# Kernel tuning notes

Measured on AMD Instinct MI355X. Metric: run time of the kernel, lower is better.

Reference implementation:

```python
import jax, jax.numpy as jnp
import numpy as np

B, V, FIN, H = 200, 40, 16, 128
NSW = 12          # switch edges
NE = 40           # regular edges
M = NE + NSW      # 52 total edges
MLP_HID = 1024
OUT = M + V + NSW # 104


def _build_graph():
    rng = np.random.default_rng(0)
    pairs = set()
    while len(pairs) < M:
        i, j = map(int, rng.integers(0, V, 2))
        if i < j:
            pairs.add((i, j))
    pairs = sorted(pairs)
    reg = np.array(pairs[:NE], np.int64)   # (NE,2)
    sw = np.array(pairs[NE:], np.int64)    # (NSW,2) row-major sorted, matches torch.nonzero order
    edges = np.concatenate([reg, sw], 0)   # switch edges last, matching graph_topo layout
    A = np.zeros((V, M), np.float32)
    A[edges[:, 0], np.arange(M)] = 1.0
    A[edges[:, 1], np.arange(M)] = -1.0
    return reg, sw, A


def setup_inputs():
    key = jax.random.key(0)
    ks = jax.random.split(key, 16)
    reg, sw, A = _build_graph()
    ei = jnp.broadcast_to(jnp.asarray(reg.T)[None], (B, 2, NE))
    si = jnp.broadcast_to(jnp.asarray(sw.T)[None], (B, 2, NSW))

    def w(k, shp, fan):
        return jax.random.normal(k, shp, jnp.float32) / np.sqrt(fan)

    return {
        'x_mod': jax.random.normal(ks[0], (B, V, FIN), jnp.float32),
        'ei': ei, 'si': si, 'A_inc': jnp.asarray(A),
        'embed': w(ks[1], (2, FIN), 1.0),
        'WU0': w(ks[2], (FIN, H), FIN), 'WV0': w(ks[3], (FIN, H), FIN),
        'WA0': w(ks[4], (FIN, H), FIN), 'WB0': w(ks[5], (FIN, H), FIN),
        'WC0': w(ks[6], (FIN, H), FIN),
        'WU1': w(ks[7], (H, H), H), 'WV1': w(ks[8], (H, H), H),
        'WA1': w(ks[9], (H, H), H), 'WB1': w(ks[10], (H, H), H),
        'WC1': w(ks[11], (H, H), H),
        'W1': w(ks[12], ((NSW + V) * H, MLP_HID), (NSW + V) * H),
        'b1': jnp.zeros((MLP_HID,), jnp.float32),
        'W2': w(ks[13], (MLP_HID, OUT), MLP_HID),
        'b2': jnp.zeros((OUT,), jnp.float32),
    }


def _layer(x, s, adj, smask, WU, WV, WA, WB, WC, residual):
    Ux = x @ WU
    Vx = x @ WV
    # gate features over dense VxV switch grid: e_ij = A s_ij + B x_i + C x_j
    e = jnp.einsum('bijf,fh->bijh', s, WA) + (x @ WB)[:, :, None, :] + (x @ WC)[:, None, :, :]
    gates = jax.nn.sigmoid(e) * smask[..., None]
    msg_edges = jnp.einsum('bij,bjh->bih', adj, Vx)   # regular-edge aggregation
    msg_sw = jnp.einsum('bijh,bjh->bih', gates, Vx)   # gated switch aggregation
    xh = jax.nn.relu(Ux + msg_edges + msg_sw)
    sh = jax.nn.relu(e)
    if residual:
        xh = x + xh
        sh = s + sh
    return xh, sh


def reference(x_mod, ei, si, A_inc, embed, WU0, WV0, WA0, WB0, WC0,
              WU1, WV1, WA1, WB1, WC1, W1, b1, W2, b2):
    i_sw, j_sw = si[0, 0], si[0, 1]   # switch indices (shared across batch)
    i_e, j_e = ei[0, 0], ei[0, 1]
    S = jnp.zeros((V, V), bool).at[i_sw, j_sw].set(True)   # upper-tri switch mask
    smask = jnp.broadcast_to(S, (B, V, V)).astype(x_mod.dtype)
    s0 = embed[S.astype(jnp.int32)]                        # (V,V,FIN) edge embedding
    s = jnp.broadcast_to(s0[None], (B, V, V, FIN))
    adj1 = jnp.zeros((V, V), x_mod.dtype).at[i_e, j_e].set(1.0)
    adj = jnp.broadcast_to((adj1 + adj1.T)[None], (B, V, V))
    x, s = _layer(x_mod, s, adj, smask, WU0, WV0, WA0, WB0, WC0, residual=False)
    x, s = _layer(x, s, adj, smask, WU1, WV1, WA1, WB1, WC1, residual=True)
    switches = s[:, i_sw, j_sw, :]                         # (B,NSW,H) irregular gather (torch.nonzero path)
    mlp_in = jnp.concatenate([switches.reshape(B, -1), x.reshape(B, -1)], axis=1)
    out = jax.nn.relu(mlp_in @ W1 + b1) @ W2 + b2          # (B,OUT)
    p_switch = jax.nn.sigmoid(out[:, -NSW:])
    graph_topo = jnp.ones((B, M), out.dtype).at[:, M - NSW:].set(p_switch)
    v = out[:, M:M + V].at[:, 0].set(1.0)
    p_fc = graph_topo * out[:, :M]
    q_fc = graph_topo * (v @ A_inc)                        # per-edge voltage difference flow
    pg = x_mod[:, :, 0] + jnp.einsum('vm,bm->bv', A_inc, p_fc)  # power balance completion
    qg = x_mod[:, :, 1] + jnp.einsum('vm,bm->bv', A_inc, q_fc)
    z = jnp.concatenate([p_fc, v, graph_topo], axis=1)     # (B, 2M+V)
    zc = jnp.concatenate([q_fc, pg, qg], axis=1)           # (B, M+2V)
    return z, zc
```

## Files before the change

kernel.cpp:

```cpp
#include <hip/hip_runtime.h>
#include <math.h>

#define B       200
#define V       40
#define FIN     16
#define H       128
#define NSW     12
#define NE      40
#define M       52
#define MLP_HID 1024
#define OUTD    104
#define MLP_IN  6656
#define ZDIM    144
#define ZCDIM   132
#define NCH     13
#define X1LD    136

typedef __attribute__((ext_vector_type(8))) short bf16x8;
typedef __attribute__((ext_vector_type(4))) float f32x4;

__device__ __forceinline__ float sigmoidf(float x) {
    return 1.0f / (1.0f + expf(-x));
}
__device__ __forceinline__ unsigned short f2b(float x) {
    unsigned int u = __float_as_uint(x);
    u += 0x7fffu + ((u >> 16) & 1u);
    return (unsigned short)(u >> 16);
}
__device__ __forceinline__ float b2f(unsigned short s) {
    return __uint_as_float(((unsigned int)s) << 16);
}

__global__ __launch_bounds__(256) void k_prep(const float* __restrict__ W1,
        const float* __restrict__ WU, const float* __restrict__ WV,
        const float* __restrict__ WB, const float* __restrict__ WC,
        const float* __restrict__ W2,
        unsigned short* __restrict__ W1t, unsigned short* __restrict__ Wt512,
        unsigned short* __restrict__ W2t) {
    int tid = threadIdx.x;
    if (blockIdx.x < 208) {
        int k0 = blockIdx.x * 32, n0 = blockIdx.y * 32;
        __shared__ float tile[32][33];
        int c = tid & 31, r8 = tid >> 5;
#pragma unroll
        for (int i = 0; i < 4; ++i) {
            int r = r8 + i * 8;
            tile[r][c] = W1[(size_t)(k0 + r) * MLP_HID + n0 + c];
        }
        __syncthreads();
#pragma unroll
        for (int i = 0; i < 4; ++i) {
            int rr = r8 + i * 8;
            W1t[(size_t)(n0 + rr) * MLP_IN + k0 + c] = f2b(tile[c][rr]);
        }
    } else if (blockIdx.x == 208) {
        int base = (blockIdx.y * 256 + tid) * 8;
#pragma unroll
        for (int i = 0; i < 8; ++i) {
            int o = base + i;
            int col = o >> 7, f = o & 127;
            int m = col >> 7, h = col & 127;
            const float* Ws = (m == 0) ? WU : (m == 1) ? WV : (m == 2) ? WB : WC;
            Wt512[o] = f2b(Ws[f * H + h]);
        }
    } else {
        for (int o = blockIdx.y * 4096 + tid; o < blockIdx.y * 4096 + 4096; o += 256) {
            int col = o >> 10, k = o & 1023;
            W2t[o] = (col < OUTD) ? f2b(W2[(size_t)k * OUTD + col]) : (unsigned short)0;
        }
    }
}

__global__ __launch_bounds__(512) void k_gnn(const float* __restrict__ x,
        const int* __restrict__ ei, const int* __restrict__ si,
        const float* __restrict__ embed,
        const float* __restrict__ WU0, const float* __restrict__ WV0,
        const float* __restrict__ WB0, const float* __restrict__ WC0,
        const float* __restrict__ WA0, const float* __restrict__ WA1,
        const unsigned short* __restrict__ Wt512,
        unsigned short* __restrict__ Abf) {
    int b = blockIdx.x;
    int tid = threadIdx.x;
    __shared__ unsigned short uvbc[V * 512];
    __shared__ float msg[4][V][H];
    __shared__ unsigned short x1l[48 * X1LD];
    __shared__ unsigned short e0s[NSW * H];
    __shared__ float xs[V * FIN];
    __shared__ float sA1l[NSW * H];

    for (int i = tid; i < V * FIN; i += 512) xs[i] = x[(size_t)b * V * FIN + i];
    __syncthreads();

    int h = tid & 127, sub = tid >> 7;

    {
        int m = sub;
        const float* Wm = (m == 0) ? WU0 : (m == 1) ? WV0 : (m == 2) ? WB0 : WC0;
        float w[FIN];
#pragma unroll
        for (int f = 0; f < FIN; ++f) w[f] = Wm[f * H + h];
        for (int r = 0; r < V; ++r) {
            float acc = 0.f;
#pragma unroll
            for (int f = 0; f < FIN; ++f) acc += xs[r * FIN + f] * w[f];
            uvbc[r * 512 + tid] = f2b(acc);
        }
    }
    for (int i = 0; i < V; ++i) msg[sub][i][h] = 0.f;
    __syncthreads();

    float sA0 = 0.f;
#pragma unroll
    for (int f = 0; f < FIN; ++f) sA0 += embed[FIN + f] * WA0[f * H + h];

    for (int e = sub * 10; e < sub * 10 + 10; ++e) {
        int i = ei[e], j = ei[NE + e];
        msg[sub][i][h] += b2f(uvbc[j * 512 + 128 + h]);
        msg[sub][j][h] += b2f(uvbc[i * 512 + 128 + h]);
    }
    for (int k = sub * 3; k < sub * 3 + 3; ++k) {
        int i = si[k], j = si[NSW + k];
        float e0 = sA0 + b2f(uvbc[i * 512 + 256 + h]) + b2f(uvbc[j * 512 + 384 + h]);
        float g = sigmoidf(e0);
        msg[sub][i][h] += g * b2f(uvbc[j * 512 + 128 + h]);
        e0s[k * H + h] = f2b(fmaxf(e0, 0.f));
    }
    __syncthreads();

    for (int i = sub * 10; i < sub * 10 + 10; ++i) {
        float v = b2f(uvbc[i * 512 + h]) + msg[0][i][h] + msg[1][i][h] + msg[2][i][h] + msg[3][i][h];
        x1l[i * X1LD + h] = f2b(fmaxf(v, 0.f));
    }
    for (int i = 40 + sub; i < 48; i += 4) x1l[i * X1LD + h] = 0;
    for (int o = tid; o < NSW * H; o += 512) {
        int k = o >> 7, hh = o & 127;
        float acc = 0.f;
#pragma unroll 8
        for (int f = 0; f < H; ++f) acc += b2f(e0s[k * H + f]) * WA1[f * H + hh];
        sA1l[o] = acc;
    }
    __syncthreads();

    {
        int lane = tid & 63, wvid = tid >> 6;
        int n0w = wvid * 64;
        int lr = lane & 15, lk = lane >> 4;
        f32x4 acc[3][4];
#pragma unroll
        for (int rf = 0; rf < 3; ++rf)
#pragma unroll
            for (int cf = 0; cf < 4; ++cf) acc[rf][cf] = (f32x4){0.f, 0.f, 0.f, 0.f};

#pragma unroll
        for (int kk = 0; kk < 4; ++kk) {
            int kseg = kk * 32 + lk * 8;
            bf16x8 af0 = *(const bf16x8*)&x1l[(0 * 16 + lr) * X1LD + kseg];
            bf16x8 af1 = *(const bf16x8*)&x1l[(1 * 16 + lr) * X1LD + kseg];
            bf16x8 af2 = *(const bf16x8*)&x1l[(2 * 16 + lr) * X1LD + kseg];
#pragma unroll
            for (int cf = 0; cf < 4; ++cf) {
                int col = n0w + cf * 16 + lr;
                bf16x8 bf = *(const bf16x8*)&Wt512[col * 128 + kseg];
                acc[0][cf] = __builtin_amdgcn_mfma_f32_16x16x32_bf16(af0, bf, acc[0][cf], 0, 0, 0);
                acc[1][cf] = __builtin_amdgcn_mfma_f32_16x16x32_bf16(af1, bf, acc[1][cf], 0, 0, 0);
                acc[2][cf] = __builtin_amdgcn_mfma_f32_16x16x32_bf16(af2, bf, acc[2][cf], 0, 0, 0);
            }
        }
#pragma unroll
        for (int rf = 0; rf < 3; ++rf)
#pragma unroll
            for (int cf = 0; cf < 4; ++cf)
#pragma unroll
                for (int r = 0; r < 4; ++r) {
                    int row = rf * 16 + lk * 4 + r;
                    if (row < V) uvbc[row * 512 + n0w + cf * 16 + lr] = f2b(acc[rf][cf][r]);
                }
    }
    for (int i = 0; i < V; ++i) msg[sub][i][h] = 0.f;
    __syncthreads();

    for (int e = sub * 10; e < sub * 10 + 10; ++e) {
        int i = ei[e], j = ei[NE + e];
        msg[sub][i][h] += b2f(uvbc[j * 512 + 128 + h]);
        msg[sub][j][h] += b2f(uvbc[i * 512 + 128 + h]);
    }
    for (int k = sub * 3; k < sub * 3 + 3; ++k) {
        int i = si[k], j = si[NSW + k];
        float e1 = sA1l[k * H + h] + b2f(uvbc[i * 512 + 256 + h]) + b2f(uvbc[j * 512 + 384 + h]);
        float g = sigmoidf(e1);
        msg[sub][i][h] += g * b2f(uvbc[j * 512 + 128 + h]);
        float s1 = b2f(e0s[k * H + h]);
        Abf[(size_t)b * MLP_IN + k * H + h] = f2b(s1 + fmaxf(e1, 0.f));
    }
    __syncthreads();
    for (int i = sub * 10; i < sub * 10 + 10; ++i) {
        float xh = b2f(uvbc[i * 512 + h]) + msg[0][i][h] + msg[1][i][h] + msg[2][i][h] + msg[3][i][h];
        float x2 = b2f(x1l[i * X1LD + h]) + fmaxf(xh, 0.f);
        Abf[(size_t)b * MLP_IN + NSW * H + i * H + h] = f2b(x2);
    }
}

template<int MODE>
__global__ __launch_bounds__(256) void k_gemm(const unsigned short* __restrict__ A,
        const unsigned short* __restrict__ Bt, void* __restrict__ Cout,
        int K, int nk, int ldc) {
    int tid = threadIdx.x;
    int lane = tid & 63, wv = tid >> 6;
    int wr = (wv >> 1) * 32, wc = (wv & 1) * 32;
    int n0 = blockIdx.x * 64, m0 = blockIdx.y * 64;
    size_t kbase = (size_t)blockIdx.z * nk * 32;

    __shared__ __align__(16) unsigned short a_lds[64 * 40];
    __shared__ __align__(16) unsigned short b_lds[64 * 40];

    f32x4 acc00 = {0,0,0,0}, acc01 = {0,0,0,0}, acc10 = {0,0,0,0}, acc11 = {0,0,0,0};

    int srow = tid >> 2, sseg = tid & 3;
    const int4* gA = (const int4*)(A + (size_t)(m0 + srow) * K + kbase + sseg * 8);
    const int4* gB = (const int4*)(Bt + (size_t)(n0 + srow) * K + kbase + sseg * 8);
    int lws = srow * 40 + sseg * 8;

    int a_off = (wr + (lane & 15)) * 40 + (lane >> 4) * 8;
    int b_off = (wc + (lane & 15)) * 40 + (lane >> 4) * 8;

    int4 ra = gA[0], rb = gB[0];
    for (int kk = 0; kk < nk; ++kk) {
        *(int4*)&a_lds[lws] = ra;
        *(int4*)&b_lds[lws] = rb;
        __syncthreads();
        if (kk + 1 < nk) { ra = gA[(kk + 1) * 4]; rb = gB[(kk + 1) * 4]; }
        bf16x8 a0 = *(const bf16x8*)&a_lds[a_off];
        bf16x8 a1 = *(const bf16x8*)&a_lds[a_off + 16 * 40];
        bf16x8 b0 = *(const bf16x8*)&b_lds[b_off];
        bf16x8 b1 = *(const bf16x8*)&b_lds[b_off + 16 * 40];
        acc00 = __builtin_amdgcn_mfma_f32_16x16x32_bf16(a0, b0, acc00, 0, 0, 0);
        acc01 = __builtin_amdgcn_mfma_f32_16x16x32_bf16(a0, b1, acc01, 0, 0, 0);
        acc10 = __builtin_amdgcn_mfma_f32_16x16x32_bf16(a1, b0, acc10, 0, 0, 0);
        acc11 = __builtin_amdgcn_mfma_f32_16x16x32_bf16(a1, b1, acc11, 0, 0, 0);
        __syncthreads();
    }

    int crow = (lane >> 4) * 4;
    int ccol = lane & 15;
    int row0 = m0 + wr + crow, row1 = row0 + 16;
    int col0 = n0 + wc + ccol, col1 = col0 + 16;
    if (MODE == 1) {
        unsigned short* dst = (unsigned short*)Cout;
#pragma unroll
        for (int r = 0; r < 4; ++r) {
            dst[(size_t)(row0 + r) * ldc + col0] = f2b(acc00[r]);
            dst[(size_t)(row0 + r) * ldc + col1] = f2b(acc01[r]);
            dst[(size_t)(row1 + r) * ldc + col0] = f2b(acc10[r]);
            dst[(size_t)(row1 + r) * ldc + col1] = f2b(acc11[r]);
        }
    } else {
        float* dst = (float*)Cout + (size_t)blockIdx.z * (gridDim.y * 64) * ldc;
#pragma unroll
        for (int r = 0; r < 4; ++r) {
            dst[(size_t)(row0 + r) * ldc + col0] = acc00[r];
            dst[(size_t)(row0 + r) * ldc + col1] = acc01[r];
            dst[(size_t)(row1 + r) * ldc + col0] = acc10[r];
            dst[(size_t)(row1 + r) * ldc + col1] = acc11[r];
        }
    }
}

__global__ void k_mred(const float* __restrict__ partial, const float* __restrict__ b1,
                       unsigned short* __restrict__ hiddenb) {
    int i = blockIdx.x * 256 + threadIdx.x;
    float s = b1[i & (MLP_HID - 1)];
#pragma unroll
    for (int z = 0; z < NCH; ++z) s += partial[(size_t)z * 256 * MLP_HID + i];
    hiddenb[i] = f2b(fmaxf(s, 0.f));
}

__global__ __launch_bounds__(128) void k_fin(const float* __restrict__ partial2,
        const float* __restrict__ b2, const float* __restrict__ A,
        const float* __restrict__ x_mod, float* __restrict__ outp) {
    int b = blockIdx.x;
    int tid = threadIdx.x;
    __shared__ float o[OUTD];
    __shared__ float gt[M], vv[V], pfc[M], qfc[M];

    if (tid < OUTD) {
        float s = b2[tid];
#pragma unroll
        for (int z = 0; z < 4; ++z) s += partial2[(size_t)z * 256 * 128 + b * 128 + tid];
        o[tid] = s;
    }
    __syncthreads();

    if (tid < M) {
        float g = (tid < M - NSW) ? 1.0f : sigmoidf(o[M + V + (tid - (M - NSW))]);
        gt[tid] = g;
        pfc[tid] = g * o[tid];
    }
    if (tid < V) vv[tid] = (tid == 0) ? 1.0f : o[M + tid];
    __syncthreads();

    if (tid < M) {
        float acc = 0.f;
        for (int x = 0; x < V; ++x) acc += vv[x] * A[x * M + tid];
        qfc[tid] = gt[tid] * acc;
    }
    __syncthreads();

    float* zb = outp + (size_t)b * ZDIM;
    if (tid < M) zb[tid] = pfc[tid];
    if (tid < V) zb[M + tid] = vv[tid];
    if (tid < M) zb[M + V + tid] = gt[tid];

    float* zcb = outp + (size_t)B * ZDIM + (size_t)b * ZCDIM;
    if (tid < M) zcb[tid] = qfc[tid];
    if (tid < V) {
        float accp = 0.f, accq = 0.f;
        for (int m = 0; m < M; ++m) {
            float a = A[tid * M + m];
            accp += a * pfc[m];
            accq += a * qfc[m];
        }
        zcb[M + tid]     = x_mod[(size_t)(b * V + tid) * FIN + 0] + accp;
        zcb[M + V + tid] = x_mod[(size_t)(b * V + tid) * FIN + 1] + accq;
    }
}

extern "C" void kernel_launch(void* const* d_in, const int* in_sizes, int n_in,
                              void* d_out, int out_size, void* d_ws, size_t ws_size,
                              hipStream_t stream) {
    const float* x_mod = (const float*)d_in[0];
    const int*   ei    = (const int*)d_in[1];
    const int*   si    = (const int*)d_in[2];
    const float* A     = (const float*)d_in[3];
    const float* embed = (const float*)d_in[4];
    const float* WU0   = (const float*)d_in[5];
    const float* WV0   = (const float*)d_in[6];
    const float* WA0   = (const float*)d_in[7];
    const float* WB0   = (const float*)d_in[8];
    const float* WC0   = (const float*)d_in[9];
    const float* WU1   = (const float*)d_in[10];
    const float* WV1   = (const float*)d_in[11];
    const float* WA1   = (const float*)d_in[12];
    const float* WB1   = (const float*)d_in[13];
    const float* WC1   = (const float*)d_in[14];
    const float* W1    = (const float*)d_in[15];
    const float* b1    = (const float*)d_in[16];
    const float* W2    = (const float*)d_in[17];
    const float* b2    = (const float*)d_in[18];
    float* out = (float*)d_out;

    char* ws = (char*)d_ws;
    unsigned short* W1t      = (unsigned short*)(ws + 0);
    unsigned short* Wt512    = (unsigned short*)(ws + 13631488);
    unsigned short* W2t      = (unsigned short*)(ws + 13762560);
    unsigned short* Abf      = (unsigned short*)(ws + 14024704);
    float*          partialM = (float*)(ws + 17432576);
    unsigned short* hiddenb  = (unsigned short*)(ws + 31064064);
    float*          partial2 = (float*)(ws + 31588352);

    k_prep<<<dim3(210, 32), 256, 0, stream>>>(W1, WU1, WV1, WB1, WC1, W2, W1t, Wt512, W2t);
    k_gnn<<<B, 512, 0, stream>>>(x_mod, ei, si, embed, WU0, WV0, WB0, WC0, WA0, WA1,
                                 Wt512, Abf);
    k_gemm<2><<<dim3(16, 4, NCH), 256, 0, stream>>>(Abf, W1t, partialM, MLP_IN, 16, MLP_HID);
    k_mred<<<256 * MLP_HID / 256, 256, 0, stream>>>(partialM, b1, hiddenb);
    k_gemm<2><<<dim3(2, 4, 4), 256, 0, stream>>>(hiddenb, W2t, partial2, MLP_HID, 8, 128);
    k_fin<<<B, 128, 0, stream>>>(partial2, b2, A, x_mod, out);
}
```

Baseline: 66.22 us.

## Read fp32 W1 directly in MLP GEMM and restructure GNN with adjacency lists and MFMA

Result: faster. 56.48 us (-14.7%).

```diff
diff --git a/kernel.cpp b/kernel.cpp
--- a/kernel.cpp
+++ b/kernel.cpp
@@ -15,6 +15,7 @@
 #define ZCDIM   132
 #define NCH     13
 #define X1LD    136
+#define MAXD    16
 
 typedef __attribute__((ext_vector_type(8))) short bf16x8;
 typedef __attribute__((ext_vector_type(4))) float f32x4;
@@ -31,140 +32,102 @@
     return __uint_as_float(((unsigned int)s) << 16);
 }
 
-__global__ __launch_bounds__(256) void k_prep(const float* __restrict__ W1,
-        const float* __restrict__ WU, const float* __restrict__ WV,
-        const float* __restrict__ WB, const float* __restrict__ WC,
-        const float* __restrict__ W2,
-        unsigned short* __restrict__ W1t, unsigned short* __restrict__ Wt512,
+__global__ __launch_bounds__(256) void k_prep(
+        const float* __restrict__ WU0, const float* __restrict__ WV0,
+        const float* __restrict__ WB0, const float* __restrict__ WC0,
+        const float* __restrict__ WU1, const float* __restrict__ WV1,
+        const float* __restrict__ WB1, const float* __restrict__ WC1,
+        const float* __restrict__ WA1, const float* __restrict__ W2,
+        unsigned short* __restrict__ W0t, unsigned short* __restrict__ Wt640,
         unsigned short* __restrict__ W2t) {
-    int tid = threadIdx.x;
-    if (blockIdx.x < 208) {
-        int k0 = blockIdx.x * 32, n0 = blockIdx.y * 32;
-        __shared__ float tile[32][33];
-        int c = tid & 31, r8 = tid >> 5;
-#pragma unroll
-        for (int i = 0; i < 4; ++i) {
-            int r = r8 + i * 8;
-            tile[r][c] = W1[(size_t)(k0 + r) * MLP_HID + n0 + c];
-        }
-        __syncthreads();
-#pragma unroll
-        for (int i = 0; i < 4; ++i) {
-            int rr = r8 + i * 8;
-            W1t[(size_t)(n0 + rr) * MLP_IN + k0 + c] = f2b(tile[c][rr]);
-        }
-    } else if (blockIdx.x == 208) {
-        int base = (blockIdx.y * 256 + tid) * 8;
+    int bx = blockIdx.x, tid = threadIdx.x;
+    if (bx < 64) {
+        int o0 = bx * 2048 + tid * 8;
 #pragma unroll
         for (int i = 0; i < 8; ++i) {
-            int o = base + i;
-            int col = o >> 7, f = o & 127;
-            int m = col >> 7, h = col & 127;
-            const float* Ws = (m == 0) ? WU : (m == 1) ? WV : (m == 2) ? WB : WC;
-            Wt512[o] = f2b(Ws[f * H + h]);
+            int o = o0 + i; int col = o >> 10, k = o & 1023;
+            W2t[o] = (col < OUTD) ? f2b(W2[(size_t)k * OUTD + col]) : (unsigned short)0;
+        }
+    } else if (bx < 104) {
+        int o0 = (bx - 64) * 2048 + tid * 8;
+#pragma unroll
+        for (int i = 0; i < 8; ++i) {
+            int o = o0 + i; int col = o >> 7, f = o & 127;
+            int m = col >> 7, hh = col & 127;
+            const float* Ws = (m == 0) ? WU1 : (m == 1) ? WV1 : (m == 2) ? WB1
+                            : (m == 3) ? WC1 : WA1;
+            Wt640[o] = f2b(Ws[f * H + hh]);
         }
     } else {
-        for (int o = blockIdx.y * 4096 + tid; o < blockIdx.y * 4096 + 4096; o += 256) {
-            int col = o >> 10, k = o & 1023;
-            W2t[o] = (col < OUTD) ? f2b(W2[(size_t)k * OUTD + col]) : (unsigned short)0;
+        int o0 = (bx - 104) * 2048 + tid * 8;
+#pragma unroll
+        for (int i = 0; i < 8; ++i) {
+            int o = o0 + i; int col = o >> 5, k = o & 31;
+            int m = col >> 7, hh = col & 127;
+            const float* Ws = (m == 0) ? WU0 : (m == 1) ? WV0 : (m == 2) ? WB0 : WC0;
+            W0t[o] = (k < FIN) ? f2b(Ws[k * H + hh]) : (unsigned short)0;
         }
     }
 }
 
 __global__ __launch_bounds__(512) void k_gnn(const float* __restrict__ x,
         const int* __restrict__ ei, const int* __restrict__ si,
-        const float* __restrict__ embed,
-        const float* __restrict__ WU0, const float* __restrict__ WV0,
-        const float* __restrict__ WB0, const float* __restrict__ WC0,
-        const float* __restrict__ WA0, const float* __restrict__ WA1,
-        const unsigned short* __restrict__ Wt512,
+        const float* __restrict__ embed, const float* __restrict__ WA0,
+        const unsigned short* __restrict__ W0t,
+        const unsigned short* __restrict__ Wt640,
         unsigned short* __restrict__ Abf) {
-    int b = blockIdx.x;
-    int tid = threadIdx.x;
+    int b = blockIdx.x, tid = threadIdx.x;
+    __shared__ unsigned short xb[48 * 40];
     __shared__ unsigned short uvbc[V * 512];
-    __shared__ float msg[4][V][H];
-    __shared__ unsigned short x1l[48 * X1LD];
-    __shared__ unsigned short e0s[NSW * H];
-    __shared__ float xs[V * FIN];
+    __shared__ unsigned short x1l[64 * X1LD];
+    __shared__ float gL[NSW * H];
     __shared__ float sA1l[NSW * H];
-
-    for (int i = tid; i < V * FIN; i += 512) xs[i] = x[(size_t)b * V * FIN + i];
-    __syncthreads();
+    __shared__ int   nbr[V][MAXD];
+    __shared__ int   deg[V];
 
     int h = tid & 127, sub = tid >> 7;
-
+    int lane = tid & 63, wv = tid >> 6;
+    int lr = lane & 15, lk = lane >> 4;
+    int n0w = wv * 64;
+
+    for (int o = tid; o < 48 * 32; o += 512) {
+        int r = o >> 5, k = o & 31;
+        float v = (r < V && k < FIN) ? x[(size_t)b * V * FIN + r * FIN + k] : 0.f;
+        xb[r * 40 + k] = f2b(v);
+    }
+    if (tid < V) deg[tid] = 0;
+    for (int o = tid; o < 12 * 128; o += 512) {
+        int rr = o >> 7;
+        int row = (rr < 8) ? 40 + rr : 60 + (rr - 8);
+        x1l[row * X1LD + (o & 127)] = 0;
+    }
+    __syncthreads();
+
+    if (tid < NE) {
+        int i = ei[tid], j = ei[NE + tid];
+        int p = atomicAdd(&deg[i], 1); if (p < MAXD) nbr[i][p] = j;
+        int q = atomicAdd(&deg[j], 1); if (q < MAXD) nbr[j][q] = i;
+    } else if (tid < NE + NSW) {
+        int k = tid - NE;
+        int i = si[k], j = si[NSW + k];
+        int p = atomicAdd(&deg[i], 1); if (p < MAXD) nbr[i][p] = j | ((k + 1) << 8);
+    }
     {
-        int m = sub;
-        const float* Wm = (m == 0) ? WU0 : (m == 1) ? WV0 : (m == 2) ? WB0 : WC0;
-        float w[FIN];
-#pragma unroll
-        for (int f = 0; f < FIN; ++f) w[f] = Wm[f * H + h];
-        for (int r = 0; r < V; ++r) {
-            float acc = 0.f;
-#pragma unroll
-            for (int f = 0; f < FIN; ++f) acc += xs[r * FIN + f] * w[f];
-            uvbc[r * 512 + tid] = f2b(acc);
-        }
-    }
-    for (int i = 0; i < V; ++i) msg[sub][i][h] = 0.f;
-    __syncthreads();
-
-    float sA0 = 0.f;
-#pragma unroll
-    for (int f = 0; f < FIN; ++f) sA0 += embed[FIN + f] * WA0[f * H + h];
-
-    for (int e = sub * 10; e < sub * 10 + 10; ++e) {
-        int i = ei[e], j = ei[NE + e];
-        msg[sub][i][h] += b2f(uvbc[j * 512 + 128 + h]);
-        msg[sub][j][h] += b2f(uvbc[i * 512 + 128 + h]);
-    }
-    for (int k = sub * 3; k < sub * 3 + 3; ++k) {
-        int i = si[k], j = si[NSW + k];
-        float e0 = sA0 + b2f(uvbc[i * 512 + 256 + h]) + b2f(uvbc[j * 512 + 384 + h]);
-        float g = sigmoidf(e0);
-        msg[sub][i][h] += g * b2f(uvbc[j * 512 + 128 + h]);
-        e0s[k * H + h] = f2b(fmaxf(e0, 0.f));
-    }
-    __syncthreads();
-
-    for (int i = sub * 10; i < sub * 10 + 10; ++i) {
-        float v = b2f(uvbc[i * 512 + h]) + msg[0][i][h] + msg[1][i][h] + msg[2][i][h] + msg[3][i][h];
-        x1l[i * X1LD + h] = f2b(fmaxf(v, 0.f));
-    }
-    for (int i = 40 + sub; i < 48; i += 4) x1l[i * X1LD + h] = 0;
-    for (int o = tid; o < NSW * H; o += 512) {
-        int k = o >> 7, hh = o & 127;
-        float acc = 0.f;
-#pragma unroll 8
-        for (int f = 0; f < H; ++f) acc += b2f(e0s[k * H + f]) * WA1[f * H + hh];
-        sA1l[o] = acc;
-    }
-    __syncthreads();
-
-    {
-        int lane = tid & 63, wvid = tid >> 6;
-        int n0w = wvid * 64;
-        int lr = lane & 15, lk = lane >> 4;
         f32x4 acc[3][4];
 #pragma unroll
         for (int rf = 0; rf < 3; ++rf)
 #pragma unroll
             for (int cf = 0; cf < 4; ++cf) acc[rf][cf] = (f32x4){0.f, 0.f, 0.f, 0.f};
-
-#pragma unroll
-        for (int kk = 0; kk < 4; ++kk) {
-            int kseg = kk * 32 + lk * 8;
-            bf16x8 af0 = *(const bf16x8*)&x1l[(0 * 16 + lr) * X1LD + kseg];
-            bf16x8 af1 = *(const bf16x8*)&x1l[(1 * 16 + lr) * X1LD + kseg];
-            bf16x8 af2 = *(const bf16x8*)&x1l[(2 * 16 + lr) * X1LD + kseg];
-#pragma unroll
-            for (int cf = 0; cf < 4; ++cf) {
-                int col = n0w + cf * 16 + lr;
-                bf16x8 bf = *(const bf16x8*)&Wt512[col * 128 + kseg];
-                acc[0][cf] = __builtin_amdgcn_mfma_f32_16x16x32_bf16(af0, bf, acc[0][cf], 0, 0, 0);
-                acc[1][cf] = __builtin_amdgcn_mfma_f32_16x16x32_bf16(af1, bf, acc[1][cf], 0, 0, 0);
-                acc[2][cf] = __builtin_amdgcn_mfma_f32_16x16x32_bf16(af2, bf, acc[2][cf], 0, 0, 0);
-            }
+        int kseg = lk * 8;
+        bf16x8 a0 = *(const bf16x8*)&xb[lr * 40 + kseg];
+        bf16x8 a1 = *(const bf16x8*)&xb[(16 + lr) * 40 + kseg];
+        bf16x8 a2 = *(const bf16x8*)&xb[(32 + lr) * 40 + kseg];
+#pragma unroll
+        for (int cf = 0; cf < 4; ++cf) {
+            bf16x8 bf = *(const bf16x8*)&W0t[(n0w + cf * 16 + lr) * 32 + kseg];
+            acc[0][cf] = __builtin_amdgcn_mfma_f32_16x16x32_bf16(a0, bf, acc[0][cf], 0, 0, 0);
+            acc[1][cf] = __builtin_amdgcn_mfma_f32_16x16x32_bf16(a1, bf, acc[1][cf], 0, 0, 0);
+            acc[2][cf] = __builtin_amdgcn_mfma_f32_16x16x32_bf16(a2, bf, acc[2][cf], 0, 0, 0);
         }
 #pragma unroll
         for (int rf = 0; rf < 3; ++rf)
@@ -176,27 +139,163 @@
                     if (row < V) uvbc[row * 512 + n0w + cf * 16 + lr] = f2b(acc[rf][cf][r]);
                 }
     }
-    for (int i = 0; i < V; ++i) msg[sub][i][h] = 0.f;
-    __syncthreads();
-
-    for (int e = sub * 10; e < sub * 10 + 10; ++e) {
-        int i = ei[e], j = ei[NE + e];
-        msg[sub][i][h] += b2f(uvbc[j * 512 + 128 + h]);
-        msg[sub][j][h] += b2f(uvbc[i * 512 + 128 + h]);
-    }
-    for (int k = sub * 3; k < sub * 3 + 3; ++k) {
+    __syncthreads();
+
+    {
+        float sA0 = 0.f;
+#pragma unroll
+        for (int f = 0; f < FIN; ++f) sA0 += embed[FIN + f] * WA0[f * H + h];
+        for (int k = sub; k < NSW; k += 4) {
+            int i = si[k], j = si[NSW + k];
+            float e0 = sA0 + b2f(uvbc[i * 512 + 256 + h]) + b2f(uvbc[j * 512 + 384 + h]);
+            gL[k * H + h] = sigmoidf(e0);
+            x1l[(48 + k) * X1LD + h] = f2b(fmaxf(e0, 0.f));
+        }
+    }
+    __syncthreads();
+
+    for (int i = sub * 10; i < sub * 10 + 10; ++i) {
+        float acc = b2f(uvbc[i * 512 + h]);
+        int d = deg[i]; if (d > MAXD) d = MAXD;
+        for (int p = 0; p < d; ++p) {
+            int ent = nbr[i][p];
+            float vv = b2f(uvbc[(ent & 255) * 512 + 128 + h]);
+            int g = ent >> 8;
+            if (g) vv *= gL[(g - 1) * H + h];
+            acc += vv;
+        }
+        x1l[i * X1LD + h] = f2b(fmaxf(acc, 0.f));
+    }
+    __syncthreads();
+
+    {
+        f32x4 acc[3][4], accs = (f32x4){0.f, 0.f, 0.f, 0.f};
+#pragma unroll
+        for (int rf = 0; rf < 3; ++rf)
+#pragma unroll
+            for (int cf = 0; cf < 4; ++cf) acc[rf][cf] = (f32x4){0.f, 0.f, 0.f, 0.f};
+#pragma unroll
+        for (int kk = 0; kk < 4; ++kk) {
+            int kseg = kk * 32 + lk * 8;
+            bf16x8 a0 = *(const bf16x8*)&x1l[lr * X1LD + kseg];
+            bf16x8 a1 = *(const bf16x8*)&x1l[(16 + lr) * X1LD + kseg];
+            bf16x8 a2 = *(const bf16x8*)&x1l[(32 + lr) * X1LD + kseg];
+            bf16x8 as = *(const bf16x8*)&x1l[(48 + lr) * X1LD + kseg];
+#pragma unroll
+            for (int cf = 0; cf < 4; ++cf) {
+                bf16x8 bf = *(const bf16x8*)&Wt640[(size_t)(n0w + cf * 16 + lr) * H + kseg];
+                acc[0][cf] = __builtin_amdgcn_mfma_f32_16x16x32_bf16(a0, bf, acc[0][cf], 0, 0, 0);
+                acc[1][cf] = __builtin_amdgcn_mfma_f32_16x16x32_bf16(a1, bf, acc[1][cf], 0, 0, 0);
+                acc[2][cf] = __builtin_amdgcn_mfma_f32_16x16x32_bf16(a2, bf, acc[2][cf], 0, 0, 0);
+            }
+            bf16x8 bs = *(const bf16x8*)&Wt640[(size_t)(512 + wv * 16 + lr) * H + kseg];
+            accs = __builtin_amdgcn_mfma_f32_16x16x32_bf16(as, bs, accs, 0, 0, 0);
+        }
+#pragma unroll
+        for (int rf = 0; rf < 3; ++rf)
+#pragma unroll
+            for (int cf = 0; cf < 4; ++cf)
+#pragma unroll
+                for (int r = 0; r < 4; ++r) {
+                    int row = rf * 16 + lk * 4 + r;
+                    if (row < V) uvbc[row * 512 + n0w + cf * 16 + lr] = f2b(acc[rf][cf][r]);
+                }
+#pragma unroll
+        for (int r = 0; r < 4; ++r) {
+            int sr = lk * 4 + r;
+            if (sr < NSW) sA1l[sr * H + wv * 16 + lr] = accs[r];
+        }
+    }
+    __syncthreads();
+
+    for (int k = sub; k < NSW; k += 4) {
         int i = si[k], j = si[NSW + k];
         float e1 = sA1l[k * H + h] + b2f(uvbc[i * 512 + 256 + h]) + b2f(uvbc[j * 512 + 384 + h]);
-        float g = sigmoidf(e1);
-        msg[sub][i][h] += g * b2f(uvbc[j * 512 + 128 + h]);
-        float s1 = b2f(e0s[k * H + h]);
+        gL[k * H + h] = sigmoidf(e1);
+        float s1 = b2f(x1l[(48 + k) * X1LD + h]);
         Abf[(size_t)b * MLP_IN + k * H + h] = f2b(s1 + fmaxf(e1, 0.f));
     }
     __syncthreads();
+
     for (int i = sub * 10; i < sub * 10 + 10; ++i) {
-        float xh = b2f(uvbc[i * 512 + h]) + msg[0][i][h] + msg[1][i][h] + msg[2][i][h] + msg[3][i][h];
-        float x2 = b2f(x1l[i * X1LD + h]) + fmaxf(xh, 0.f);
+        float acc = b2f(uvbc[i * 512 + h]);
+        int d = deg[i]; if (d > MAXD) d = MAXD;
+        for (int p = 0; p < d; ++p) {
+            int ent = nbr[i][p];
+            float vv = b2f(uvbc[(ent & 255) * 512 + 128 + h]);
+            int g = ent >> 8;
+            if (g) vv *= gL[(g - 1) * H + h];
+            acc += vv;
+        }
+        float x2 = b2f(x1l[i * X1LD + h]) + fmaxf(acc, 0.f);
         Abf[(size_t)b * MLP_IN + NSW * H + i * H + h] = f2b(x2);
+    }
+}
+
+__global__ __launch_bounds__(256) void k_mlp(const unsigned short* __restrict__ A,
+        const float* __restrict__ W1, float* __restrict__ partial) {
+    const int NK = 16;
+    int tid = threadIdx.x;
+    int lane = tid & 63, wvv = tid >> 6;
+    int wr = (wvv >> 1) * 32, wc = (wvv & 1) * 32;
+    int n0 = blockIdx.x * 64, m0 = blockIdx.y * 64;
+    int kbase = blockIdx.z * NK * 32;
+
+    __shared__ __align__(16) unsigned short a_lds[64 * 40];
+    __shared__ __align__(16) unsigned short b_lds[64 * 40];
+
+    f32x4 acc00 = {0,0,0,0}, acc01 = {0,0,0,0}, acc10 = {0,0,0,0}, acc11 = {0,0,0,0};
+
+    int srow = tid >> 2, sseg = tid & 3;
+    const int4* gA = (const int4*)(A + (size_t)(m0 + srow) * MLP_IN + kbase + sseg * 8);
+    int lwsA = srow * 40 + sseg * 8;
+
+    int bcol = tid & 63, bkg = tid >> 6;
+    const float* gW = W1 + (size_t)(kbase + bkg * 8) * MLP_HID + n0 + bcol;
+    int lwsB = bcol * 40 + bkg * 8;
+
+    int a_off = (wr + (lane & 15)) * 40 + (lane >> 4) * 8;
+    int b_off = (wc + (lane & 15)) * 40 + (lane >> 4) * 8;
+
+    int4 ra = gA[0];
+    float rfv[8];
+#pragma unroll
+    for (int i = 0; i < 8; ++i) rfv[i] = gW[(size_t)i * MLP_HID];
+
+    for (int kk = 0; kk < NK; ++kk) {
+        *(int4*)&a_lds[lwsA] = ra;
+        union { unsigned short us[8]; int4 v; } pk;
+#pragma unroll
+        for (int i = 0; i < 8; ++i) pk.us[i] = f2b(rfv[i]);
+        *(int4*)&b_lds[lwsB] = pk.v;
+        __syncthreads();
+        if (kk + 1 < NK) {
+            ra = gA[(kk + 1) * 4];
+            const float* g2 = gW + (size_t)(kk + 1) * 32 * MLP_HID;
+#pragma unroll
+            for (int i = 0; i < 8; ++i) rfv[i] = g2[(size_t)i * MLP_HID];
+        }
+        bf16x8 a0 = *(const bf16x8*)&a_lds[a_off];
+        bf16x8 a1 = *(const bf16x8*)&a_lds[a_off + 16 * 40];
+        bf16x8 b0 = *(const bf16x8*)&b_lds[b_off];
+        bf16x8 b1 = *(const bf16x8*)&b_lds[b_off + 16 * 40];
+        acc00 = __builtin_amdgcn_mfma_f32_16x16x32_bf16(a0, b0, acc00, 0, 0, 0);
+        acc01 = __builtin_amdgcn_mfma_f32_16x16x32_bf16(a0, b1, acc01, 0, 0, 0);
+        acc10 = __builtin_amdgcn_mfma_f32_16x16x32_bf16(a1, b0, acc10, 0, 0, 0);
+        acc11 = __builtin_amdgcn_mfma_f32_16x16x32_bf16(a1, b1, acc11, 0, 0, 0);
+        __syncthreads();
+    }
+
+    int crow = (lane >> 4) * 4, ccol = lane & 15;
+    int row0 = m0 + wr + crow, row1 = row0 + 16;
+    int col0 = n0 + wc + ccol, col1 = col0 + 16;
+    float* dst = partial + (size_t)blockIdx.z * 256 * MLP_HID;
+#pragma unroll
+    for (int r = 0; r < 4; ++r) {
+        dst[(size_t)(row0 + r) * MLP_HID + col0] = acc00[r];
+        dst[(size_t)(row0 + r) * MLP_HID + col1] = acc01[r];
+        dst[(size_t)(row1 + r) * MLP_HID + col0] = acc10[r];
+        dst[(size_t)(row1 + r) * MLP_HID + col1] = acc11[r];
     }
 }
 
@@ -240,28 +339,16 @@
         __syncthreads();
     }
 
-    int crow = (lane >> 4) * 4;
-    int ccol = lane & 15;
+    int crow = (lane >> 4) * 4, ccol = lane & 15;
     int row0 = m0 + wr + crow, row1 = row0 + 16;
     int col0 = n0 + wc + ccol, col1 = col0 + 16;
-    if (MODE == 1) {
-        unsigned short* dst = (unsigned short*)Cout;
-#pragma unroll
-        for (int r = 0; r < 4; ++r) {
-            dst[(size_t)(row0 + r) * ldc + col0] = f2b(acc00[r]);
-            dst[(size_t)(row0 + r) * ldc + col1] = f2b(acc01[r]);
-            dst[(size_t)(row1 + r) * ldc + col0] = f2b(acc10[r]);
-            dst[(size_t)(row1 + r) * ldc + col1] = f2b(acc11[r]);
-        }
-    } else {
-        float* dst = (float*)Cout + (size_t)blockIdx.z * (gridDim.y * 64) * ldc;
-#pragma unroll
-        for (int r = 0; r < 4; ++r) {
-            dst[(size_t)(row0 + r) * ldc + col0] = acc00[r];
-            dst[(size_t)(row0 + r) * ldc + col1] = acc01[r];
-            dst[(size_t)(row1 + r) * ldc + col0] = acc10[r];
-            dst[(size_t)(row1 + r) * ldc + col1] = acc11[r];
-        }
+    float* dst = (float*)Cout + (size_t)blockIdx.z * (gridDim.y * 64) * ldc;
+#pragma unroll
+    for (int r = 0; r < 4; ++r) {
+        dst[(size_t)(row0 + r) * ldc + col0] = acc00[r];
+        dst[(size_t)(row0 + r) * ldc + col1] = acc01[r];
+        dst[(size_t)(row1 + r) * ldc + col0] = acc10[r];
+        dst[(size_t)(row1 + r) * ldc + col1] = acc11[r];
     }
 }
 
@@ -349,18 +436,18 @@
     float* out = (float*)d_out;
 
     char* ws = (char*)d_ws;
-    unsigned short* W1t      = (unsigned short*)(ws + 0);
-    unsigned short* Wt512    = (unsigned short*)(ws + 13631488);
-    unsigned short* W2t      = (unsigned short*)(ws + 13762560);
-    unsigned short* Abf      = (unsigned short*)(ws + 14024704);
-    float*          partialM = (float*)(ws + 17432576);
-    unsigned short* hiddenb  = (unsigned short*)(ws + 31064064);
-    float*          partial2 = (float*)(ws + 31588352);
-
-    k_prep<<<dim3(210, 32), 256, 0, stream>>>(W1, WU1, WV1, WB1, WC1, W2, W1t, Wt512, W2t);
-    k_gnn<<<B, 512, 0, stream>>>(x_mod, ei, si, embed, WU0, WV0, WB0, WC0, WA0, WA1,
-                                 Wt512, Abf);
-    k_gemm<2><<<dim3(16, 4, NCH), 256, 0, stream>>>(Abf, W1t, partialM, MLP_IN, 16, MLP_HID);
+    unsigned short* W0t      = (unsigned short*)(ws + 0);
+    unsigned short* Wt640    = (unsigned short*)(ws + 32768);
+    unsigned short* W2t      = (unsigned short*)(ws + 196608);
+    unsigned short* Abf      = (unsigned short*)(ws + 458752);
+    float*          partialM = (float*)(ws + 3866624);
+    unsigned short* hiddenb  = (unsigned short*)(ws + 17498112);
+    float*          partial2 = (float*)(ws + 18022400);
+
+    k_prep<<<112, 256, 0, stream>>>(WU0, WV0, WB0, WC0, WU1, WV1, WB1, WC1, WA1, W2,
+                                    W0t, Wt640, W2t);
+    k_gnn<<<B, 512, 0, stream>>>(x_mod, ei, si, embed, WA0, W0t, Wt640, Abf);
+    k_mlp<<<dim3(16, 4, NCH), 256, 0, stream>>>(Abf, W1, partialM);
     k_mred<<<256 * MLP_HID / 256, 256, 0, stream>>>(partialM, b1, hiddenb);
     k_gemm<2><<<dim3(2, 4, 4), 256, 0, stream>>>(hiddenb, W2t, partial2, MLP_HID, 8, 128);
     k_fin<<<B, 128, 0, stream>>>(partial2, b2, A, x_mod, out);
```
